# Performance work log

Hardware: AMD Instinct MI355X
Metric: run time of the kernel (lower is better)

The kernel has to match this reference:

```python
import jax, jax.numpy as jnp
import numpy as np


def _forward_algorithm(emissions, mask, start, end, trans, reverse):
    """emissions: (B, L, T), mask: (B, L) -> log probs (L, B, T)."""
    em = jnp.transpose(emissions, (1, 0, 2))          # (L, B, T)
    m = jnp.transpose(mask.astype(em.dtype), (1, 0))  # (L, B)
    B, T = em.shape[1], em.shape[2]
    if not reverse:
        init = em[0] + start[None, :]                 # (B, T)

        def step(prev, xs):
            e_t, m_t = xs
            # inner[b, j, k] = prev[b, j] + trans[j, k] + em_t[b, k]
            inner = prev[:, :, None] + trans[None, :, :] + e_t[:, None, :]
            new = jax.nn.logsumexp(inner, axis=1)
            new = new * m_t[:, None] + prev * (1.0 - m_t)[:, None]
            return new, new

        _, ys = jax.lax.scan(step, init, (em[1:], m[1:]))
        return jnp.concatenate([init[None], ys], axis=0)
    else:
        init = jnp.broadcast_to(end[None, :], (B, T))
        transT = trans.T

        def step(prev, xs):
            e_t, m_t = xs
            # inner[b, j, k] = prev[b, j] + trans[k, j] + em_t[b, j]
            inner = prev[:, :, None] + transT[None, :, :] + e_t[:, :, None]
            new = jax.nn.logsumexp(inner, axis=1)
            new = new * m_t[:, None] + prev * (1.0 - m_t)[:, None]
            return new, new

        # iterate i = L-1 ... 1 (reverse), result index i-1
        _, ys = jax.lax.scan(step, init, (em[1:][::-1], m[1:][::-1]))
        return jnp.concatenate([ys[::-1], init[None]], axis=0)


def setup_inputs() -> dict:
    key = jax.random.key(0)
    k1, k2, k3, k4 = jax.random.split(key, 4)
    B, L, T = 256, 1024, 64
    emissions = jax.random.normal(k1, (B, L, T), dtype=jnp.float32)
    start_transitions = jax.random.normal(k2, (T,), dtype=jnp.float32)
    end_transitions = jax.random.normal(k3, (T,), dtype=jnp.float32)
    transitions = jax.random.normal(k4, (T, T), dtype=jnp.float32)
    mask = jnp.ones((B, L), dtype=jnp.int32)
    return {
        "emissions": emissions,
        "start_transitions": start_transitions,
        "end_transitions": end_transitions,
        "transitions": transitions,
        "mask": mask,
    }


def reference(emissions, start_transitions, end_transitions, transitions, mask):
    """CRF marginal probabilities. Returns (seq_len, batch, num_tags)."""
    alpha = _forward_algorithm(emissions, mask, start_transitions,
                               end_transitions, transitions, reverse=False)
    beta = _forward_algorithm(emissions, mask, start_transitions,
                              end_transitions, transitions, reverse=True)
    z = jax.nn.logsumexp(alpha[-1] + end_transitions[None, :], axis=1)  # (B,)
    return jnp.exp(alpha + beta - z[None, :, None])
```

## Files before the change

### kernel.cpp

```cpp
#include <hip/hip_runtime.h>

#define B_ 256
#define L_ 1024
#define T_ 64

typedef float f4v __attribute__((ext_vector_type(4)));

__device__ __forceinline__ float rfl(float x) {
    return __int_as_float(__builtin_amdgcn_readfirstlane(__float_as_int(x)));
}

__global__ __launch_bounds__(64)
void crf_scan(const float* __restrict__ em, const float* __restrict__ start_t,
              const float* __restrict__ end_t, const float* __restrict__ trans,
              const int* __restrict__ mask, float* __restrict__ alpha,
              float* __restrict__ beta, float* __restrict__ zbuf)
{
    const int lane = threadIdx.x;
    const int cb = blockIdx.x;
    const bool fwd = cb < B_;
    const int b = fwd ? cb : cb - B_;

    __shared__ float shu[T_];

    float e[T_];
    if (fwd) {
#pragma unroll
        for (int j = 0; j < T_; ++j) e[j] = __expf(trans[j * T_ + lane]);
    } else {
#pragma unroll
        for (int j = 0; j < T_; ++j) e[j] = __expf(trans[lane * T_ + j]);
    }

    const float* emb = em + (size_t)b * (L_ * T_);
    const int* mb = mask + (size_t)b * L_;
    const size_t stride = (size_t)B_ * T_;

    if (fwd) {
        float st0 = emb[lane] + start_t[lane];
        float c = rfl(st0);
        float u = __expf(st0 - c);
        float* ap = alpha + (size_t)b * T_ + lane;
        __builtin_nontemporal_store(st0, ap);
        ap += stride;

        float pe0 = emb[1 * T_ + lane], pe1 = emb[2 * T_ + lane],
              pe2 = emb[3 * T_ + lane], pe3 = emb[4 * T_ + lane],
              pe4 = emb[5 * T_ + lane], pe5 = emb[6 * T_ + lane];
        int pm0 = mb[1], pm1 = mb[2], pm2 = mb[3], pm3 = mb[4],
            pm4 = mb[5], pm5 = mb[6];

        for (int t = 1; t < L_; ++t) {
            float f = __expf(pe0);
            int mv = pm0;
            pe0 = pe1; pe1 = pe2; pe2 = pe3; pe3 = pe4; pe4 = pe5;
            pm0 = pm1; pm1 = pm2; pm2 = pm3; pm3 = pm4; pm4 = pm5;
            int tn = t + 6; if (tn > L_ - 1) tn = L_ - 1;
            pe5 = emb[tn * T_ + lane];
            pm5 = mb[tn];

            shu[lane] = u;
            __builtin_amdgcn_wave_barrier();
            float u0v = rfl(u);
            float r = __builtin_amdgcn_rcpf(u0v);
            float um = u * r;
            float s = f * r;
            c = c + __logf(u0v);
            const f4v* q4 = (const f4v*)shu;
            float a0 = 0.f, a1 = 0.f, a2 = 0.f, a3 = 0.f;
#pragma unroll
            for (int j4 = 0; j4 < 16; ++j4) {
                f4v q = q4[j4];
                a0 = fmaf(q.x, e[4 * j4 + 0], a0);
                a1 = fmaf(q.y, e[4 * j4 + 1], a1);
                a2 = fmaf(q.z, e[4 * j4 + 2], a2);
                a3 = fmaf(q.w, e[4 * j4 + 3], a3);
            }
            float cand = ((a0 + a1) + (a2 + a3)) * s;
            float un = (mv != 0) ? cand : um;
            float av = c + __logf(un);
            __builtin_nontemporal_store(av, ap);
            ap += stride;
            u = un;
        }
        float v = u * __expf(end_t[lane]);
        for (int off = 32; off; off >>= 1) v += __shfl_xor(v, off);
        if (lane == 0) zbuf[b] = c + __logf(v);
    } else {
        float bv0 = end_t[lane];
        float c = rfl(bv0);
        float u = __expf(bv0 - c);
        float* bp = beta + ((size_t)(L_ - 1) * B_ + b) * T_ + lane;
        __builtin_nontemporal_store(bv0, bp);
        bp -= stride;

        float pe0 = emb[(L_ - 1) * T_ + lane], pe1 = emb[(L_ - 2) * T_ + lane],
              pe2 = emb[(L_ - 3) * T_ + lane], pe3 = emb[(L_ - 4) * T_ + lane],
              pe4 = emb[(L_ - 5) * T_ + lane], pe5 = emb[(L_ - 6) * T_ + lane];
        int pm0 = mb[L_ - 1], pm1 = mb[L_ - 2], pm2 = mb[L_ - 3],
            pm3 = mb[L_ - 4], pm4 = mb[L_ - 5], pm5 = mb[L_ - 6];

        for (int i = L_ - 1; i >= 1; --i) {
            float f = __expf(pe0);
            int mv = pm0;
            pe0 = pe1; pe1 = pe2; pe2 = pe3; pe3 = pe4; pe4 = pe5;
            pm0 = pm1; pm1 = pm2; pm2 = pm3; pm3 = pm4; pm4 = pm5;
            int tn = i - 6; if (tn < 1) tn = 1;
            pe5 = emb[tn * T_ + lane];
            pm5 = mb[tn];

            float w = u * f;
            shu[lane] = w;
            __builtin_amdgcn_wave_barrier();
            float u0v = rfl(u);
            float r = __builtin_amdgcn_rcpf(u0v);
            float um = u * r;
            c = c + __logf(u0v);
            const f4v* q4 = (const f4v*)shu;
            float a0 = 0.f, a1 = 0.f, a2 = 0.f, a3 = 0.f;
#pragma unroll
            for (int j4 = 0; j4 < 16; ++j4) {
                f4v q = q4[j4];
                a0 = fmaf(q.x, e[4 * j4 + 0], a0);
                a1 = fmaf(q.y, e[4 * j4 + 1], a1);
                a2 = fmaf(q.z, e[4 * j4 + 2], a2);
                a3 = fmaf(q.w, e[4 * j4 + 3], a3);
            }
            float cand = ((a0 + a1) + (a2 + a3)) * r;
            float un = (mv != 0) ? cand : um;
            float bvv = c + __logf(un);
            __builtin_nontemporal_store(bvv, bp);
            bp -= stride;
            u = un;
        }
    }
}

__global__ __launch_bounds__(256)
void crf_finalize(const float* __restrict__ alpha,
                  const float* __restrict__ zbuf,
                  float* __restrict__ out)
{
    size_t i4 = (size_t)blockIdx.x * blockDim.x + threadIdx.x;
    const f4v* a4 = (const f4v*)alpha;
    f4v* o4 = (f4v*)out;
    int b = (int)((i4 >> 4) & (B_ - 1));
    float z = zbuf[b];
    f4v a = __builtin_nontemporal_load(&a4[i4]);
    f4v bb = __builtin_nontemporal_load(&o4[i4]);
    f4v o;
    o.x = __expf(a.x + bb.x - z);
    o.y = __expf(a.y + bb.y - z);
    o.z = __expf(a.z + bb.z - z);
    o.w = __expf(a.w + bb.w - z);
    __builtin_nontemporal_store(o, &o4[i4]);
}

extern "C" void kernel_launch(void* const* d_in, const int* in_sizes, int n_in,
                              void* d_out, int out_size, void* d_ws, size_t ws_size,
                              hipStream_t stream) {
    const float* em = (const float*)d_in[0];
    const float* st = (const float*)d_in[1];
    const float* en = (const float*)d_in[2];
    const float* tr = (const float*)d_in[3];
    const int*   mk = (const int*)d_in[4];
    float* out   = (float*)d_out;
    float* alpha = (float*)d_ws;
    float* zbuf  = alpha + (size_t)L_ * B_ * T_;

    crf_scan<<<2 * B_, T_, 0, stream>>>(em, st, en, tr, mk, alpha, out, zbuf);
    size_t n4 = (size_t)L_ * B_ * T_ / 4;
    crf_finalize<<<(int)(n4 / 256), 256, 0, stream>>>(alpha, zbuf, out);
}
```

Before: 631.4 us.

## Broadcast scan state via readlane instead of LDS and renormalize after dot

Replaces the per-step LDS write, wave barrier and LDS vector reads with 64 v_readlane broadcasts of the state into scalar registers for the 64-wide dot product. Normalization now divides by lane 0 of the new value after the dot rather than before it, and the log-scale only advances on unmasked steps. Nontemporal stores and loads are replaced with plain ones, and launch bounds now request a minimum of one block per multiprocessor. Readlane serializes through the scalar path, so each step trades the LDS round-trip latency for 64 dependent scalar reads.

New measurement: 531.7 us. 1.19x faster.

```diff
diff --git a/kernel.cpp b/kernel.cpp
--- a/kernel.cpp
+++ b/kernel.cpp
@@ -9,8 +9,11 @@
 __device__ __forceinline__ float rfl(float x) {
     return __int_as_float(__builtin_amdgcn_readfirstlane(__float_as_int(x)));
 }
+__device__ __forceinline__ float rlane(float x, int j) {
+    return __int_as_float(__builtin_amdgcn_readlane(__float_as_int(x), j));
+}
 
-__global__ __launch_bounds__(64)
+__global__ __launch_bounds__(64, 1)
 void crf_scan(const float* __restrict__ em, const float* __restrict__ start_t,
               const float* __restrict__ end_t, const float* __restrict__ trans,
               const int* __restrict__ mask, float* __restrict__ alpha,
@@ -20,8 +23,6 @@
     const int cb = blockIdx.x;
     const bool fwd = cb < B_;
     const int b = fwd ? cb : cb - B_;
-
-    __shared__ float shu[T_];
 
     float e[T_];
     if (fwd) {
@@ -41,7 +42,7 @@
         float c = rfl(st0);
         float u = __expf(st0 - c);
         float* ap = alpha + (size_t)b * T_ + lane;
-        __builtin_nontemporal_store(st0, ap);
+        *ap = st0;
         ap += stride;
 
         float pe0 = emb[1 * T_ + lane], pe1 = emb[2 * T_ + lane],
@@ -56,30 +57,32 @@
             pe0 = pe1; pe1 = pe2; pe2 = pe3; pe3 = pe4; pe4 = pe5;
             pm0 = pm1; pm1 = pm2; pm2 = pm3; pm3 = pm4; pm4 = pm5;
             int tn = t + 6; if (tn > L_ - 1) tn = L_ - 1;
-            pe5 = emb[tn * T_ + lane];
+            pe5 = emb[(size_t)tn * T_ + lane];
             pm5 = mb[tn];
 
-            shu[lane] = u;
-            __builtin_amdgcn_wave_barrier();
-            float u0v = rfl(u);
-            float r = __builtin_amdgcn_rcpf(u0v);
-            float um = u * r;
-            float s = f * r;
-            c = c + __logf(u0v);
-            const f4v* q4 = (const f4v*)shu;
-            float a0 = 0.f, a1 = 0.f, a2 = 0.f, a3 = 0.f;
+            float um = u;
+            float acc[4] = {0.f, 0.f, 0.f, 0.f};
 #pragma unroll
-            for (int j4 = 0; j4 < 16; ++j4) {
-                f4v q = q4[j4];
-                a0 = fmaf(q.x, e[4 * j4 + 0], a0);
-                a1 = fmaf(q.y, e[4 * j4 + 1], a1);
-                a2 = fmaf(q.z, e[4 * j4 + 2], a2);
-                a3 = fmaf(q.w, e[4 * j4 + 3], a3);
+            for (int j = 0; j < 32; ++j) {
+                float uj = rlane(u, j);
+                acc[j & 3] = fmaf(uj, e[j], acc[j & 3]);
             }
-            float cand = ((a0 + a1) + (a2 + a3)) * s;
+#pragma unroll
+            for (int j = 32; j < 64; ++j) {
+                float uj = rlane(u, j);
+                acc[j & 3] = fmaf(uj, e[j], acc[j & 3]);
+            }
+            float dot = (acc[0] + acc[1]) + (acc[2] + acc[3]);
+            float d0 = rfl(dot);
+            float f0 = rfl(f);
+            float u00 = d0 * f0;
+            float r = __builtin_amdgcn_rcpf(u00);
+            float cand = (dot * f) * r;
+            float cn = c + __logf(u00);
             float un = (mv != 0) ? cand : um;
+            c = (mv != 0) ? cn : c;
             float av = c + __logf(un);
-            __builtin_nontemporal_store(av, ap);
+            *ap = av;
             ap += stride;
             u = un;
         }
@@ -91,12 +94,12 @@
         float c = rfl(bv0);
         float u = __expf(bv0 - c);
         float* bp = beta + ((size_t)(L_ - 1) * B_ + b) * T_ + lane;
-        __builtin_nontemporal_store(bv0, bp);
+        *bp = bv0;
         bp -= stride;
 
-        float pe0 = emb[(L_ - 1) * T_ + lane], pe1 = emb[(L_ - 2) * T_ + lane],
-              pe2 = emb[(L_ - 3) * T_ + lane], pe3 = emb[(L_ - 4) * T_ + lane],
-              pe4 = emb[(L_ - 5) * T_ + lane], pe5 = emb[(L_ - 6) * T_ + lane];
+        float pe0 = emb[(size_t)(L_ - 1) * T_ + lane], pe1 = emb[(size_t)(L_ - 2) * T_ + lane],
+              pe2 = emb[(size_t)(L_ - 3) * T_ + lane], pe3 = emb[(size_t)(L_ - 4) * T_ + lane],
+              pe4 = emb[(size_t)(L_ - 5) * T_ + lane], pe5 = emb[(size_t)(L_ - 6) * T_ + lane];
         int pm0 = mb[L_ - 1], pm1 = mb[L_ - 2], pm2 = mb[L_ - 3],
             pm3 = mb[L_ - 4], pm4 = mb[L_ - 5], pm5 = mb[L_ - 6];
 
@@ -106,30 +109,31 @@
             pe0 = pe1; pe1 = pe2; pe2 = pe3; pe3 = pe4; pe4 = pe5;
             pm0 = pm1; pm1 = pm2; pm2 = pm3; pm3 = pm4; pm4 = pm5;
             int tn = i - 6; if (tn < 1) tn = 1;
-            pe5 = emb[tn * T_ + lane];
+            pe5 = emb[(size_t)tn * T_ + lane];
             pm5 = mb[tn];
 
             float w = u * f;
-            shu[lane] = w;
-            __builtin_amdgcn_wave_barrier();
-            float u0v = rfl(u);
-            float r = __builtin_amdgcn_rcpf(u0v);
-            float um = u * r;
-            c = c + __logf(u0v);
-            const f4v* q4 = (const f4v*)shu;
-            float a0 = 0.f, a1 = 0.f, a2 = 0.f, a3 = 0.f;
+            float um = u;
+            float acc[4] = {0.f, 0.f, 0.f, 0.f};
 #pragma unroll
-            for (int j4 = 0; j4 < 16; ++j4) {
-                f4v q = q4[j4];
-                a0 = fmaf(q.x, e[4 * j4 + 0], a0);
-                a1 = fmaf(q.y, e[4 * j4 + 1], a1);
-                a2 = fmaf(q.z, e[4 * j4 + 2], a2);
-                a3 = fmaf(q.w, e[4 * j4 + 3], a3);
+            for (int j = 0; j < 32; ++j) {
+                float wj = rlane(w, j);
+                acc[j & 3] = fmaf(wj, e[j], acc[j & 3]);
             }
-            float cand = ((a0 + a1) + (a2 + a3)) * r;
+#pragma unroll
+            for (int j = 32; j < 64; ++j) {
+                float wj = rlane(w, j);
+                acc[j & 3] = fmaf(wj, e[j], acc[j & 3]);
+            }
+            float dot = (acc[0] + acc[1]) + (acc[2] + acc[3]);
+            float u00 = rfl(dot);
+            float r = __builtin_amdgcn_rcpf(u00);
+            float cand = dot * r;
+            float cn = c + __logf(u00);
             float un = (mv != 0) ? cand : um;
+            c = (mv != 0) ? cn : c;
             float bvv = c + __logf(un);
-            __builtin_nontemporal_store(bvv, bp);
+            *bp = bvv;
             bp -= stride;
             u = un;
         }
@@ -146,8 +150,8 @@
     f4v* o4 = (f4v*)out;
     int b = (int)((i4 >> 4) & (B_ - 1));
     float z = zbuf[b];
-    f4v a = __builtin_nontemporal_load(&a4[i4]);
-    f4v bb = __builtin_nontemporal_load(&o4[i4]);
+    f4v a = a4[i4];
+    f4v bb = o4[i4];
     f4v o;
     o.x = __expf(a.x + bb.x - z);
     o.y = __expf(a.y + bb.y - z);
```
